# Kernel optimization log

Measured on AMD Instinct MI355X. Metric: run time of the kernel, lower is better.

The kernel has to match this reference:

```python
import jax, jax.numpy as jnp
import numpy as np

B, T, DIM = 2, 2048, 2048
N_HEAD, N_GROUP = 16, 4
KV_HEAD = N_HEAD // N_GROUP
HEAD_DIM = DIM // N_HEAD


def setup_inputs() -> dict:
    key = jax.random.key(0)
    ks = jax.random.split(key, 7)
    x = jax.random.normal(ks[0], (B, T, DIM), dtype=jnp.float32)
    # rotary tables: last dim = head_dim // 2 (interleaved real/imag pairs)
    pos = jnp.arange(T, dtype=jnp.float32)[:, None]
    inv_freq = 1.0 / (10000.0 ** (jnp.arange(0, HEAD_DIM, 2, dtype=jnp.float32) / HEAD_DIM))
    angles = pos * inv_freq[None, :]  # [T, HEAD_DIM//2]
    freqs_cos = jnp.cos(angles)
    freqs_sin = jnp.sin(angles)
    scale = 0.02
    wq = jax.random.normal(ks[1], (DIM, N_HEAD * HEAD_DIM), dtype=jnp.float32) * scale
    wk = jax.random.normal(ks[2], (DIM, KV_HEAD * HEAD_DIM), dtype=jnp.float32) * scale
    wv = jax.random.normal(ks[3], (DIM, KV_HEAD * HEAD_DIM), dtype=jnp.float32) * scale
    wo = jax.random.normal(ks[4], (N_HEAD * HEAD_DIM, DIM), dtype=jnp.float32) * scale
    return {"x": x, "freqs_cos": freqs_cos, "freqs_sin": freqs_sin,
            "wq": wq, "wk": wk, "wv": wv, "wo": wo}


def _apply_rope(t, cos, sin):
    # t: [B, T, H, D]; interleaved pairs (..., -1, 2) as in torch reference
    tr = t.reshape(*t.shape[:-1], -1, 2)
    r, i = tr[..., 0], tr[..., 1]
    c = cos[None, :, None, :]  # [1, T, 1, D//2]
    s = sin[None, :, None, :]
    out = jnp.stack([r * c - i * s, r * s + i * c], axis=-1)
    return out.reshape(t.shape)


def reference(x, freqs_cos, freqs_sin, wq, wk, wv, wo):
    Bx, Tx, C = x.shape
    xq = (x @ wq).reshape(Bx, Tx, N_HEAD, HEAD_DIM)
    xk = (x @ wk).reshape(Bx, Tx, KV_HEAD, HEAD_DIM)
    xv = (x @ wv).reshape(Bx, Tx, KV_HEAD, HEAD_DIM)
    xq = _apply_rope(xq, freqs_cos, freqs_sin)
    xk = _apply_rope(xk, freqs_cos, freqs_sin)
    # repeat_kv: each kv head repeated n_group times consecutively
    xk = jnp.repeat(xk, N_GROUP, axis=2)  # [B, T, N_HEAD, D]
    xv = jnp.repeat(xv, N_GROUP, axis=2)
    scale = HEAD_DIM ** -0.5
    att = jnp.einsum('bqhd,bkhd->bhqk', xq, xk) * scale
    causal = jnp.tril(jnp.ones((Tx, Tx), dtype=bool))
    att = jnp.where(causal[None, None], att, -jnp.inf)
    att = jax.nn.softmax(att, axis=-1)
    out = jnp.einsum('bhqk,bkhd->bqhd', att, xv).reshape(Bx, Tx, N_HEAD * HEAD_DIM)
    return out @ wo
```

## Files before the change

### kernel.cpp

```cpp
#include <hip/hip_runtime.h>

#define TB 2
#define TT 2048
#define TDIM 2048
#define NHEADS 16
#define KVHEADS 4
#define HD 128

typedef unsigned short u16;
typedef unsigned int u32;
typedef __attribute__((ext_vector_type(8))) short short8;
typedef __attribute__((ext_vector_type(4))) float float4_t;

__device__ __forceinline__ float b2f(u16 u) {
    union { u32 i; float f; } v; v.i = ((u32)u) << 16; return v.f;
}
__device__ __forceinline__ u16 f2b(float f) {
    union { float f; u32 i; } v; v.f = f;
    u32 r = (v.i + 0x7FFFu + ((v.i >> 16) & 1u)) >> 16;
    return (u16)r;
}
__device__ __forceinline__ u32 fbits(float f) {
    union { float f; u32 i; } v; v.f = f; return v.i;
}

__device__ __forceinline__ void gl_lds16(const void* g, void* l) {
    __builtin_amdgcn_global_load_lds((const __attribute__((address_space(1))) void*)g,
                                     (__attribute__((address_space(3))) void*)l, 16, 0, 0);
}

template <bool F32OUT>
__global__ __launch_bounds__(256, 3)
void gemm_bt(const u16* __restrict__ A, const u16* __restrict__ BT,
             void* __restrict__ Cv, int M, int N, int K) {
    __shared__ __align__(16) u16 As[128 * 64];
    __shared__ __align__(16) u16 Bs[128 * 64];
    const int tid  = threadIdx.x;
    const int wave = tid >> 6, lane = tid & 63;
    const int quad = lane >> 4, l16 = lane & 15;
    const int wm = wave >> 1, wn = wave & 1;
    const int row0 = blockIdx.y * 128, col0 = blockIdx.x * 128;

    float4_t acc[4][4];
#pragma unroll
    for (int i = 0; i < 4; i++)
#pragma unroll
        for (int j = 0; j < 4; j++) acc[i][j] = (float4_t){0.f, 0.f, 0.f, 0.f};

    for (int kk = 0; kk < K; kk += 64) {
        __syncthreads();
#pragma unroll
        for (int i = 0; i < 4; i++) {
            int n = i * 256 + wave * 64 + lane;
            int r = n >> 3, c = (n & 7) ^ (r & 7);
            gl_lds16(A  + (size_t)(row0 + r) * K + kk + c * 8, &As[(i * 256 + wave * 64) * 8]);
            gl_lds16(BT + (size_t)(col0 + r) * K + kk + c * 8, &Bs[(i * 256 + wave * 64) * 8]);
        }
        __syncthreads();
#pragma unroll
        for (int ks = 0; ks < 2; ks++) {
            short8 af[4], bf[4];
#pragma unroll
            for (int mt = 0; mt < 4; mt++) {
                int m = wm * 64 + mt * 16 + l16;
                af[mt] = *(const short8*)&As[(m * 8 + ((ks * 4 + quad) ^ (l16 & 7))) * 8];
            }
#pragma unroll
            for (int nt = 0; nt < 4; nt++) {
                int n = wn * 64 + nt * 16 + l16;
                bf[nt] = *(const short8*)&Bs[(n * 8 + ((ks * 4 + quad) ^ (l16 & 7))) * 8];
            }
#pragma unroll
            for (int mt = 0; mt < 4; mt++)
#pragma unroll
                for (int nt = 0; nt < 4; nt++)
                    acc[mt][nt] = __builtin_amdgcn_mfma_f32_16x16x32_bf16(
                        af[mt], bf[nt], acc[mt][nt], 0, 0, 0);
        }
    }
#pragma unroll
    for (int mt = 0; mt < 4; mt++)
#pragma unroll
        for (int nt = 0; nt < 4; nt++)
#pragma unroll
            for (int r = 0; r < 4; r++) {
                int row = row0 + wm * 64 + mt * 16 + quad * 4 + r;
                int col = col0 + wn * 64 + nt * 16 + l16;
                if (F32OUT)
                    ((float*)Cv)[(size_t)row * N + col] = acc[mt][nt][r];
                else
                    ((u16*)Cv)[(size_t)row * N + col] = f2b(acc[mt][nt][r]);
            }
}

__global__ void cvt_transpose(const float* __restrict__ in, u16* __restrict__ out,
                              int rows, int cols) {
    __shared__ u16 tile[32][33];
    int c0 = blockIdx.x * 32, r0 = blockIdx.y * 32;
    int tx = threadIdx.x & 31, ty = threadIdx.x >> 5;
#pragma unroll
    for (int i = 0; i < 4; i++)
        tile[ty + i * 8][tx] = f2b(in[(size_t)(r0 + ty + i * 8) * cols + c0 + tx]);
    __syncthreads();
#pragma unroll
    for (int i = 0; i < 4; i++)
        out[(size_t)(c0 + ty + i * 8) * rows + r0 + tx] = tile[tx][ty + i * 8];
}

__global__ void cvt_bf16(const float* __restrict__ in, u16* __restrict__ out) {
    size_t i = ((size_t)blockIdx.x * 256 + threadIdx.x) * 4;
    float4 v = *(const float4*)(in + i);
    ushort4 o;
    o.x = f2b(v.x); o.y = f2b(v.y); o.z = f2b(v.z); o.w = f2b(v.w);
    *(ushort4*)(out + i) = o;
}

__global__ void transpose_v(const u16* __restrict__ QKV, u16* __restrict__ Vt) {
    int z = blockIdx.z, b = z >> 2, kv = z & 3;
    const u16* in = QKV + (size_t)b * TT * 3072 + 2560 + kv * HD;
    u16* out = Vt + (size_t)z * HD * TT;
    __shared__ u16 tile[32][33];
    int t0 = blockIdx.x * 32, d0 = blockIdx.y * 32;
    int tx = threadIdx.x & 31, ty = threadIdx.x >> 5;
#pragma unroll
    for (int i = 0; i < 4; i++)
        tile[ty + i * 8][tx] = in[(size_t)(t0 + ty + i * 8) * 3072 + d0 + tx];
    __syncthreads();
#pragma unroll
    for (int i = 0; i < 4; i++)
        out[(size_t)(d0 + ty + i * 8) * TT + t0 + tx] = tile[tx][ty + i * 8];
}

__global__ void rope_k(u16* __restrict__ buf, const float* __restrict__ cosb,
                       const float* __restrict__ sinb, int colbase, int ncshift,
                       int rowstride) {
    size_t gid = (size_t)blockIdx.x * 256 + threadIdx.x;
    size_t e = gid * 8;
    int ncols = 1 << ncshift;
    int row = (int)(e >> ncshift);
    int col = (int)(e & (ncols - 1));
    int i0 = (col & (HD - 1)) >> 1;
    int t = row & (TT - 1);
    u16* p = buf + (size_t)row * rowstride + colbase + col;
    union { uint4 v; u16 u[8]; } d, o;
    d.v = *(const uint4*)p;
    float4 c4 = *(const float4*)(cosb + t * 64 + i0);
    float4 s4 = *(const float4*)(sinb + t * 64 + i0);
    float cc[4] = {c4.x, c4.y, c4.z, c4.w};
    float ss[4] = {s4.x, s4.y, s4.z, s4.w};
#pragma unroll
    for (int k = 0; k < 4; k++) {
        float re = b2f(d.u[2 * k]), im = b2f(d.u[2 * k + 1]);
        o.u[2 * k]     = f2b(re * cc[k] - im * ss[k]);
        o.u[2 * k + 1] = f2b(re * ss[k] + im * cc[k]);
    }
    *(uint4*)p = o.v;
}

#define PSTR 72
__global__ __launch_bounds__(256, 2)
void attn(const u16* __restrict__ QKV, const u16* __restrict__ Vt,
          u16* __restrict__ O) {
    const int g = blockIdx.x;
    const int h = blockIdx.y;
    const int b = blockIdx.z;
    const int kvh = h >> 2;
    const int tid = threadIdx.x, w = tid >> 6, lane = tid & 63;
    const int quad = lane >> 4, l16 = lane & 15;

    __shared__ __align__(16) u16 Ks[2][64 * 128];
    __shared__ __align__(16) u16 Vs[2][128 * 64];
    __shared__ __align__(16) u16 Ps[4][16 * PSTR];

    const u16* Kbase = QKV + (size_t)b * TT * 3072 + 2048 + kvh * HD;
    const u16* Vbase = Vt + (size_t)(b * 4 + kvh) * HD * TT;
    const float Cl = 0.12753102474f;

    auto stage = [&](int kt, int bb) {
#pragma unroll
        for (int i = 0; i < 4; i++) {
            int n = i * 256 + w * 64 + lane;
            int r = n >> 4, c = (n & 15) ^ (r & 15);
            gl_lds16(Kbase + (size_t)(kt * 64 + r) * 3072 + c * 8,
                     &Ks[bb][(i * 256 + w * 64) * 8]);
        }
#pragma unroll
        for (int i = 0; i < 4; i++) {
            int n = i * 256 + w * 64 + lane;
            int d = n >> 3, c = (n & 7) ^ (d & 7);
            gl_lds16(Vbase + (size_t)d * TT + kt * 64 + c * 8,
                     &Vs[bb][(i * 256 + w * 64) * 8]);
        }
    };

    for (int ph = 0; ph < 2; ph++) {
        const int qb = ph ? (31 - g) : g;
        __syncthreads();
        stage(0, 0);

        const u16* Qrow = QKV + ((size_t)b * TT + qb * 64 + w * 16 + l16) * 3072 + h * HD;
        short8 qf[4];
#pragma unroll
        for (int ks = 0; ks < 4; ks++)
            qf[ks] = *(const short8*)(Qrow + ks * 32 + quad * 8);

        float4_t o[8];
#pragma unroll
        for (int i = 0; i < 8; i++) o[i] = (float4_t){0.f, 0.f, 0.f, 0.f};
        float mi = -1e30f, li = 0.f;
        const int qg = qb * 64 + w * 16 + l16;

        for (int kt = 0; kt <= qb; kt++) {
            const int cur = kt & 1;
            __syncthreads();
            if (kt < qb) stage(kt + 1, cur ^ 1);

            float4_t st[4];
#pragma unroll
            for (int nt = 0; nt < 4; nt++) st[nt] = (float4_t){0.f, 0.f, 0.f, 0.f};
#pragma unroll
            for (int ks = 0; ks < 4; ks++) {
                short8 af[4];
#pragma unroll
                for (int nt = 0; nt < 4; nt++)
                    af[nt] = *(const short8*)&Ks[cur][((nt * 16 + l16) * 16 +
                                                      ((ks * 4 + quad) ^ l16)) * 8];
#pragma unroll
                for (int nt = 0; nt < 4; nt++)
                    st[nt] = __builtin_amdgcn_mfma_f32_16x16x32_bf16(
                        af[nt], qf[ks], st[nt], 0, 0, 0);
            }

            if (kt == qb) {
#pragma unroll
                for (int nt = 0; nt < 4; nt++)
#pragma unroll
                    for (int r = 0; r < 4; r++) {
                        int key = kt * 64 + nt * 16 + quad * 4 + r;
                        if (key > qg) st[nt][r] = -3e38f;
                    }
            }
            float pm = -3e38f;
#pragma unroll
            for (int nt = 0; nt < 4; nt++)
#pragma unroll
                for (int r = 0; r < 4; r++) pm = fmaxf(pm, st[nt][r]);
            pm = fmaxf(pm, __shfl_xor(pm, 16, 64));
            pm = fmaxf(pm, __shfl_xor(pm, 32, 64));
            float mnew = fmaxf(mi, pm);
            float alpha = __builtin_amdgcn_exp2f((mi - mnew) * Cl);
            mi = mnew;
            const float mC = mnew * Cl;
            float rs = 0.f;
#pragma unroll
            for (int nt = 0; nt < 4; nt++)
#pragma unroll
                for (int r = 0; r < 4; r++) {
                    float e = __builtin_amdgcn_exp2f(fmaf(st[nt][r], Cl, -mC));
                    st[nt][r] = e;
                    rs += e;
                }
            rs += __shfl_xor(rs, 16, 64);
            rs += __shfl_xor(rs, 32, 64);
            li = li * alpha + rs;

#pragma unroll
            for (int nt = 0; nt < 4; nt++) {
                uint2 pk;
                pk.x = __builtin_amdgcn_perm(fbits(st[nt][1]), fbits(st[nt][0]), 0x07060302u);
                pk.y = __builtin_amdgcn_perm(fbits(st[nt][3]), fbits(st[nt][2]), 0x07060302u);
                *(uint2*)&Ps[w][l16 * PSTR + nt * 16 + quad * 4] = pk;
            }
            float a_o[4];
#pragma unroll
            for (int r = 0; r < 4; r++) a_o[r] = __shfl(alpha, quad * 4 + r, 64);
#pragma unroll
            for (int n2 = 0; n2 < 8; n2++)
#pragma unroll
                for (int r = 0; r < 4; r++) o[n2][r] *= a_o[r];

#pragma unroll
            for (int ks2 = 0; ks2 < 2; ks2++) {
                short8 ap = *(const short8*)&Ps[w][l16 * PSTR + ks2 * 32 + quad * 8];
#pragma unroll
                for (int n2 = 0; n2 < 8; n2++) {
                    short8 bv = *(const short8*)&Vs[cur][((n2 * 16 + l16) * 8 +
                                                         ((ks2 * 4 + quad) ^ (l16 & 7))) * 8];
                    o[n2] = __builtin_amdgcn_mfma_f32_16x16x32_bf16(ap, bv, o[n2], 0, 0, 0);
                }
            }
        }

        float l_o[4];
#pragma unroll
        for (int r = 0; r < 4; r++) l_o[r] = __shfl(li, quad * 4 + r, 64);
        u16* Ob2 = O + ((size_t)b * TT + qb * 64 + w * 16) * TDIM + h * HD;
#pragma unroll
        for (int n2 = 0; n2 < 8; n2++)
#pragma unroll
            for (int r = 0; r < 4; r++)
                Ob2[(size_t)(quad * 4 + r) * TDIM + n2 * 16 + l16] =
                    f2b(o[n2][r] / l_o[r]);
    }
}

extern "C" void kernel_launch(void* const* d_in, const int* in_sizes, int n_in,
                              void* d_out, int out_size, void* d_ws, size_t ws_size,
                              hipStream_t stream) {
    const float* x  = (const float*)d_in[0];
    const float* fc = (const float*)d_in[1];
    const float* fs = (const float*)d_in[2];
    const float* wq = (const float*)d_in[3];
    const float* wk = (const float*)d_in[4];
    const float* wv = (const float*)d_in[5];
    const float* wo = (const float*)d_in[6];
    float* out = (float*)d_out;

    char* ws = (char*)d_ws;
    size_t off = 0;
    auto alloc = [&](size_t bytes) -> void* {
        void* p = ws + off;
        off += (bytes + 255) & ~(size_t)255;
        return p;
    };
    u16* xb  = (u16*)alloc((size_t)4096 * 2048 * 2);
    u16* WT  = (u16*)alloc((size_t)3072 * 2048 * 2);
    u16* woT = (u16*)alloc((size_t)2048 * 2048 * 2);
    u16* QKV = (u16*)alloc((size_t)4096 * 3072 * 2);
    u16* Vtb = (u16*)alloc((size_t)4096 * 512 * 2);
    u16* Ob  = (u16*)alloc((size_t)4096 * 2048 * 2);

    dim3 blk(256);
    cvt_bf16<<<dim3(8192), blk, 0, stream>>>(x, xb);
    cvt_transpose<<<dim3(64, 64), blk, 0, stream>>>(wq, WT, 2048, 2048);
    cvt_transpose<<<dim3(16, 64), blk, 0, stream>>>(wk, WT + (size_t)2048 * 2048, 2048, 512);
    cvt_transpose<<<dim3(16, 64), blk, 0, stream>>>(wv, WT + (size_t)2560 * 2048, 2048, 512);
    cvt_transpose<<<dim3(64, 64), blk, 0, stream>>>(wo, woT, 2048, 2048);
    gemm_bt<false><<<dim3(24, 32), blk, 0, stream>>>(xb, WT, QKV, 4096, 3072, 2048);
    rope_k<<<dim3(4096), blk, 0, stream>>>(QKV, fc, fs, 0, 11, 3072);
    rope_k<<<dim3(1024), blk, 0, stream>>>(QKV, fc, fs, 2048, 9, 3072);
    transpose_v<<<dim3(64, 4, 8), blk, 0, stream>>>(QKV, Vtb);
    attn<<<dim3(16, 16, 2), blk, 0, stream>>>(QKV, Vtb, Ob);
    gemm_bt<true><<<dim3(16, 32), blk, 0, stream>>>(Ob, woT, out, 4096, 2048, 2048);
}
```

Baseline: 300.4 us.

## Fuse RoPE into QKV GEMM epilogue and process two heads per attention block

```diff
diff --git a/kernel.cpp b/kernel.cpp
--- a/kernel.cpp
+++ b/kernel.cpp
@@ -29,10 +29,11 @@
                                      (__attribute__((address_space(3))) void*)l, 16, 0, 0);
 }
 
-template <bool F32OUT>
+template <bool F32OUT, bool ROPE>
 __global__ __launch_bounds__(256, 3)
 void gemm_bt(const u16* __restrict__ A, const u16* __restrict__ BT,
-             void* __restrict__ Cv, int M, int N, int K) {
+             void* __restrict__ Cv, int M, int N, int K,
+             const float* __restrict__ fc, const float* __restrict__ fs) {
     __shared__ __align__(16) u16 As[128 * 64];
     __shared__ __align__(16) u16 Bs[128 * 64];
     const int tid  = threadIdx.x;
@@ -78,6 +79,7 @@
                         af[mt], bf[nt], acc[mt][nt], 0, 0, 0);
         }
     }
+    const bool do_rope = ROPE && (col0 < 2560);
 #pragma unroll
     for (int mt = 0; mt < 4; mt++)
 #pragma unroll
@@ -86,10 +88,18 @@
             for (int r = 0; r < 4; r++) {
                 int row = row0 + wm * 64 + mt * 16 + quad * 4 + r;
                 int col = col0 + wn * 64 + nt * 16 + l16;
+                float v = acc[mt][nt][r];
+                if (ROPE && do_rope) {
+                    float other = __shfl_xor(v, 1, 64);
+                    int t = row & (TT - 1);
+                    int i0 = (col & (HD - 1)) >> 1;
+                    float c = fc[t * 64 + i0], s = fs[t * 64 + i0];
+                    v = (col & 1) ? fmaf(v, c, other * s) : fmaf(v, c, -other * s);
+                }
                 if (F32OUT)
-                    ((float*)Cv)[(size_t)row * N + col] = acc[mt][nt][r];
+                    ((float*)Cv)[(size_t)row * N + col] = v;
                 else
-                    ((u16*)Cv)[(size_t)row * N + col] = f2b(acc[mt][nt][r]);
+                    ((u16*)Cv)[(size_t)row * N + col] = f2b(v);
             }
 }
 
@@ -131,46 +141,21 @@
         out[(size_t)(d0 + ty + i * 8) * TT + t0 + tx] = tile[tx][ty + i * 8];
 }
 
-__global__ void rope_k(u16* __restrict__ buf, const float* __restrict__ cosb,
-                       const float* __restrict__ sinb, int colbase, int ncshift,
-                       int rowstride) {
-    size_t gid = (size_t)blockIdx.x * 256 + threadIdx.x;
-    size_t e = gid * 8;
-    int ncols = 1 << ncshift;
-    int row = (int)(e >> ncshift);
-    int col = (int)(e & (ncols - 1));
-    int i0 = (col & (HD - 1)) >> 1;
-    int t = row & (TT - 1);
-    u16* p = buf + (size_t)row * rowstride + colbase + col;
-    union { uint4 v; u16 u[8]; } d, o;
-    d.v = *(const uint4*)p;
-    float4 c4 = *(const float4*)(cosb + t * 64 + i0);
-    float4 s4 = *(const float4*)(sinb + t * 64 + i0);
-    float cc[4] = {c4.x, c4.y, c4.z, c4.w};
-    float ss[4] = {s4.x, s4.y, s4.z, s4.w};
-#pragma unroll
-    for (int k = 0; k < 4; k++) {
-        float re = b2f(d.u[2 * k]), im = b2f(d.u[2 * k + 1]);
-        o.u[2 * k]     = f2b(re * cc[k] - im * ss[k]);
-        o.u[2 * k + 1] = f2b(re * ss[k] + im * cc[k]);
-    }
-    *(uint4*)p = o.v;
-}
-
 #define PSTR 72
-__global__ __launch_bounds__(256, 2)
+__global__ __launch_bounds__(256, 1)
 void attn(const u16* __restrict__ QKV, const u16* __restrict__ Vt,
           u16* __restrict__ O) {
-    const int g = blockIdx.x;
-    const int h = blockIdx.y;
-    const int b = blockIdx.z;
-    const int kvh = h >> 2;
+    const int g  = blockIdx.x;
+    const int yp = blockIdx.y;
+    const int b  = blockIdx.z;
+    const int kvh = yp >> 1;
+    const int hb  = kvh * 4 + (yp & 1) * 2;
     const int tid = threadIdx.x, w = tid >> 6, lane = tid & 63;
     const int quad = lane >> 4, l16 = lane & 15;
 
     __shared__ __align__(16) u16 Ks[2][64 * 128];
     __shared__ __align__(16) u16 Vs[2][128 * 64];
-    __shared__ __align__(16) u16 Ps[4][16 * PSTR];
+    __shared__ __align__(16) u16 Ps[8][16 * PSTR];
 
     const u16* Kbase = QKV + (size_t)b * TT * 3072 + 2048 + kvh * HD;
     const u16* Vbase = Vt + (size_t)(b * 4 + kvh) * HD * TT;
@@ -198,16 +183,22 @@
         __syncthreads();
         stage(0, 0);
 
-        const u16* Qrow = QKV + ((size_t)b * TT + qb * 64 + w * 16 + l16) * 3072 + h * HD;
-        short8 qf[4];
-#pragma unroll
-        for (int ks = 0; ks < 4; ks++)
-            qf[ks] = *(const short8*)(Qrow + ks * 32 + quad * 8);
-
-        float4_t o[8];
-#pragma unroll
-        for (int i = 0; i < 8; i++) o[i] = (float4_t){0.f, 0.f, 0.f, 0.f};
-        float mi = -1e30f, li = 0.f;
+        short8 qf[2][4];
+#pragma unroll
+        for (int hd = 0; hd < 2; hd++) {
+            const u16* Qrow = QKV + ((size_t)b * TT + qb * 64 + w * 16 + l16) * 3072
+                              + (hb + hd) * HD;
+#pragma unroll
+            for (int ks = 0; ks < 4; ks++)
+                qf[hd][ks] = *(const short8*)(Qrow + ks * 32 + quad * 8);
+        }
+
+        float4_t o[2][8];
+#pragma unroll
+        for (int hd = 0; hd < 2; hd++)
+#pragma unroll
+            for (int i = 0; i < 8; i++) o[hd][i] = (float4_t){0.f, 0.f, 0.f, 0.f};
+        float mi[2] = {-1e30f, -1e30f}, li[2] = {0.f, 0.f};
         const int qg = qb * 64 + w * 16 + l16;
 
         for (int kt = 0; kt <= qb; kt++) {
@@ -215,9 +206,11 @@
             __syncthreads();
             if (kt < qb) stage(kt + 1, cur ^ 1);
 
-            float4_t st[4];
-#pragma unroll
-            for (int nt = 0; nt < 4; nt++) st[nt] = (float4_t){0.f, 0.f, 0.f, 0.f};
+            float4_t st[2][4];
+#pragma unroll
+            for (int hd = 0; hd < 2; hd++)
+#pragma unroll
+                for (int nt = 0; nt < 4; nt++) st[hd][nt] = (float4_t){0.f, 0.f, 0.f, 0.f};
 #pragma unroll
             for (int ks = 0; ks < 4; ks++) {
                 short8 af[4];
@@ -226,81 +219,94 @@
                     af[nt] = *(const short8*)&Ks[cur][((nt * 16 + l16) * 16 +
                                                       ((ks * 4 + quad) ^ l16)) * 8];
 #pragma unroll
+                for (int nt = 0; nt < 4; nt++) {
+                    st[0][nt] = __builtin_amdgcn_mfma_f32_16x16x32_bf16(
+                        af[nt], qf[0][ks], st[0][nt], 0, 0, 0);
+                    st[1][nt] = __builtin_amdgcn_mfma_f32_16x16x32_bf16(
+                        af[nt], qf[1][ks], st[1][nt], 0, 0, 0);
+                }
+            }
+
+            const bool diag = (kt == qb);
+            float alpha[2];
+#pragma unroll
+            for (int hd = 0; hd < 2; hd++) {
+                if (diag) {
+#pragma unroll
+                    for (int nt = 0; nt < 4; nt++)
+#pragma unroll
+                        for (int r = 0; r < 4; r++) {
+                            int key = kt * 64 + nt * 16 + quad * 4 + r;
+                            if (key > qg) st[hd][nt][r] = -3e38f;
+                        }
+                }
+                float pm = -3e38f;
+#pragma unroll
                 for (int nt = 0; nt < 4; nt++)
-                    st[nt] = __builtin_amdgcn_mfma_f32_16x16x32_bf16(
-                        af[nt], qf[ks], st[nt], 0, 0, 0);
-            }
-
-            if (kt == qb) {
+#pragma unroll
+                    for (int r = 0; r < 4; r++) pm = fmaxf(pm, st[hd][nt][r]);
+                pm = fmaxf(pm, __shfl_xor(pm, 16, 64));
+                pm = fmaxf(pm, __shfl_xor(pm, 32, 64));
+                float mnew = fmaxf(mi[hd], pm);
+                alpha[hd] = __builtin_amdgcn_exp2f((mi[hd] - mnew) * Cl);
+                mi[hd] = mnew;
+                const float mC = mnew * Cl;
+                float rs = 0.f;
 #pragma unroll
                 for (int nt = 0; nt < 4; nt++)
 #pragma unroll
                     for (int r = 0; r < 4; r++) {
-                        int key = kt * 64 + nt * 16 + quad * 4 + r;
-                        if (key > qg) st[nt][r] = -3e38f;
+                        float e = __builtin_amdgcn_exp2f(fmaf(st[hd][nt][r], Cl, -mC));
+                        st[hd][nt][r] = e;
+                        rs += e;
                     }
-            }
-            float pm = -3e38f;
-#pragma unroll
-            for (int nt = 0; nt < 4; nt++)
-#pragma unroll
-                for (int r = 0; r < 4; r++) pm = fmaxf(pm, st[nt][r]);
-            pm = fmaxf(pm, __shfl_xor(pm, 16, 64));
-            pm = fmaxf(pm, __shfl_xor(pm, 32, 64));
-            float mnew = fmaxf(mi, pm);
-            float alpha = __builtin_amdgcn_exp2f((mi - mnew) * Cl);
-            mi = mnew;
-            const float mC = mnew * Cl;
-            float rs = 0.f;
-#pragma unroll
-            for (int nt = 0; nt < 4; nt++)
-#pragma unroll
-                for (int r = 0; r < 4; r++) {
-                    float e = __builtin_amdgcn_exp2f(fmaf(st[nt][r], Cl, -mC));
-                    st[nt][r] = e;
-                    rs += e;
-                }
-            rs += __shfl_xor(rs, 16, 64);
-            rs += __shfl_xor(rs, 32, 64);
-            li = li * alpha + rs;
-
-#pragma unroll
-            for (int nt = 0; nt < 4; nt++) {
-                uint2 pk;
-                pk.x = __builtin_amdgcn_perm(fbits(st[nt][1]), fbits(st[nt][0]), 0x07060302u);
-                pk.y = __builtin_amdgcn_perm(fbits(st[nt][3]), fbits(st[nt][2]), 0x07060302u);
-                *(uint2*)&Ps[w][l16 * PSTR + nt * 16 + quad * 4] = pk;
-            }
-            float a_o[4];
-#pragma unroll
-            for (int r = 0; r < 4; r++) a_o[r] = __shfl(alpha, quad * 4 + r, 64);
-#pragma unroll
-            for (int n2 = 0; n2 < 8; n2++)
-#pragma unroll
-                for (int r = 0; r < 4; r++) o[n2][r] *= a_o[r];
+                rs += __shfl_xor(rs, 16, 64);
+                rs += __shfl_xor(rs, 32, 64);
+                li[hd] = li[hd] * alpha[hd] + rs;
+
+#pragma unroll
+                for (int nt = 0; nt < 4; nt++) {
+                    uint2 pk;
+                    pk.x = __builtin_amdgcn_perm(fbits(st[hd][nt][1]), fbits(st[hd][nt][0]), 0x07060302u);
+                    pk.y = __builtin_amdgcn_perm(fbits(st[hd][nt][3]), fbits(st[hd][nt][2]), 0x07060302u);
+                    *(uint2*)&Ps[w * 2 + hd][l16 * PSTR + nt * 16 + quad * 4] = pk;
+                }
+                float a_o[4];
+#pragma unroll
+                for (int r = 0; r < 4; r++) a_o[r] = __shfl(alpha[hd], quad * 4 + r, 64);
+#pragma unroll
+                for (int n2 = 0; n2 < 8; n2++)
+#pragma unroll
+                    for (int r = 0; r < 4; r++) o[hd][n2][r] *= a_o[r];
+            }
 
 #pragma unroll
             for (int ks2 = 0; ks2 < 2; ks2++) {
-                short8 ap = *(const short8*)&Ps[w][l16 * PSTR + ks2 * 32 + quad * 8];
+                short8 apA = *(const short8*)&Ps[w * 2 + 0][l16 * PSTR + ks2 * 32 + quad * 8];
+                short8 apB = *(const short8*)&Ps[w * 2 + 1][l16 * PSTR + ks2 * 32 + quad * 8];
 #pragma unroll
                 for (int n2 = 0; n2 < 8; n2++) {
                     short8 bv = *(const short8*)&Vs[cur][((n2 * 16 + l16) * 8 +
                                                          ((ks2 * 4 + quad) ^ (l16 & 7))) * 8];
-                    o[n2] = __builtin_amdgcn_mfma_f32_16x16x32_bf16(ap, bv, o[n2], 0, 0, 0);
-                }
-            }
-        }
-
-        float l_o[4];
-#pragma unroll
-        for (int r = 0; r < 4; r++) l_o[r] = __shfl(li, quad * 4 + r, 64);
-        u16* Ob2 = O + ((size_t)b * TT + qb * 64 + w * 16) * TDIM + h * HD;
-#pragma unroll
-        for (int n2 = 0; n2 < 8; n2++)
-#pragma unroll
-            for (int r = 0; r < 4; r++)
-                Ob2[(size_t)(quad * 4 + r) * TDIM + n2 * 16 + l16] =
-                    f2b(o[n2][r] / l_o[r]);
+                    o[0][n2] = __builtin_amdgcn_mfma_f32_16x16x32_bf16(apA, bv, o[0][n2], 0, 0, 0);
+                    o[1][n2] = __builtin_amdgcn_mfma_f32_16x16x32_bf16(apB, bv, o[1][n2], 0, 0, 0);
+                }
+            }
+        }
+
+#pragma unroll
+        for (int hd = 0; hd < 2; hd++) {
+            float l_o[4];
+#pragma unroll
+            for (int r = 0; r < 4; r++) l_o[r] = __shfl(li[hd], quad * 4 + r, 64);
+            u16* Ob2 = O + ((size_t)b * TT + qb * 64 + w * 16) * TDIM + (hb + hd) * HD;
+#pragma unroll
+            for (int n2 = 0; n2 < 8; n2++)
+#pragma unroll
+                for (int r = 0; r < 4; r++)
+                    Ob2[(size_t)(quad * 4 + r) * TDIM + n2 * 16 + l16] =
+                        f2b(o[hd][n2][r] / l_o[r]);
+        }
     }
 }
 
@@ -336,10 +342,10 @@
     cvt_transpose<<<dim3(16, 64), blk, 0, stream>>>(wk, WT + (size_t)2048 * 2048, 2048, 512);
     cvt_transpose<<<dim3(16, 64), blk, 0, stream>>>(wv, WT + (size_t)2560 * 2048, 2048, 512);
     cvt_transpose<<<dim3(64, 64), blk, 0, stream>>>(wo, woT, 2048, 2048);
-    gemm_bt<false><<<dim3(24, 32), blk, 0, stream>>>(xb, WT, QKV, 4096, 3072, 2048);
-    rope_k<<<dim3(4096), blk, 0, stream>>>(QKV, fc, fs, 0, 11, 3072);
-    rope_k<<<dim3(1024), blk, 0, stream>>>(QKV, fc, fs, 2048, 9, 3072);
+    gemm_bt<false, true><<<dim3(24, 32), blk, 0, stream>>>(
+        xb, WT, QKV, 4096, 3072, 2048, fc, fs);
     transpose_v<<<dim3(64, 4, 8), blk, 0, stream>>>(QKV, Vtb);
-    attn<<<dim3(16, 16, 2), blk, 0, stream>>>(QKV, Vtb, Ob);
-    gemm_bt<true><<<dim3(16, 32), blk, 0, stream>>>(Ob, woT, out, 4096, 2048, 2048);
-}
+    attn<<<dim3(16, 8, 2), blk, 0, stream>>>(QKV, Vtb, Ob);
+    gemm_bt<true, false><<<dim3(16, 32), blk, 0, stream>>>(
+        Ob, woT, out, 4096, 2048, 2048, nullptr, nullptr);
+}
```

Result: slower. 321.6 us (+7.1%).
